# Kernel optimization log

Hardware: AMD Instinct MI355X
Metric: run time of the kernel (lower is better)

## Reference

```python
import jax, jax.numpy as jnp
import numpy as np

B, D_IN, H, V, T = 8192, 2048, 1024, 6, 6  # batch, enc input, hidden, total_vocab, max_length
TAU = 1.0

def setup_inputs() -> dict:
    key = jax.random.key(0)
    ks = jax.random.split(key, 16)
    s = 0.02
    return {
        "x": jax.random.normal(ks[0], (B, D_IN), jnp.float32),
        "u_noise": jax.random.uniform(ks[1], (T, B, V), jnp.float32),
        "W_enc": jax.random.normal(ks[2], (D_IN, H), jnp.float32) * s,
        "b_enc": jnp.zeros((H,), jnp.float32),
        "start_embed": jax.random.normal(ks[3], (H,), jnp.float32) * 0.01,
        "W_tok": jax.random.normal(ks[4], (V, H), jnp.float32) * s,
        "b_tok": jnp.zeros((H,), jnp.float32),
        "Wz": jax.random.normal(ks[5], (2 * H, H), jnp.float32) * s,
        "bz": jnp.zeros((H,), jnp.float32),
        "Wr": jax.random.normal(ks[6], (2 * H, H), jnp.float32) * s,
        "br": jnp.zeros((H,), jnp.float32),
        "Wh": jax.random.normal(ks[7], (2 * H, H), jnp.float32) * s,
        "bh": jnp.zeros((H,), jnp.float32),
        "W_out": jax.random.normal(ks[8], (H, V), jnp.float32) * s,
        "b_out": jnp.zeros((V,), jnp.float32),
    }

def reference(x, u_noise, W_enc, b_enc, start_embed, W_tok, b_tok,
              Wz, bz, Wr, br, Wh, bh, W_out, b_out):
    eps = 1e-10
    # uniform -> Gumbel(0,1) noise, precomputed per step: (T, B, V)
    g_all = -jnp.log(-jnp.log(u_noise + eps) + eps)
    h0 = x @ W_enc + b_enc                                   # encoder: (B, H)
    batch = x.shape[0]
    prev0 = jnp.broadcast_to(start_embed, (batch, start_embed.shape[0]))
    rc0 = jnp.ones((batch, 1), x.dtype)                      # running continue mask
    nt0 = jnp.zeros((batch,), x.dtype)                       # differentiable token count

    def step(carry, g):
        h, prev, rc, nt = carry
        nt = nt + rc[:, 0]
        comb = jnp.concatenate([prev, h], axis=-1)           # (B, 2H)
        z = jax.nn.sigmoid(comb @ Wz + bz)
        r = jax.nn.sigmoid(comb @ Wr + br)
        comb_r = jnp.concatenate([prev, r * h], axis=-1)
        h_tilde = jnp.tanh(comb_r @ Wh + bh)
        h = (1 - z) * h + z * h_tilde                        # GRU update
        logits = h @ W_out + b_out                           # (B, V)
        # hard gumbel-softmax with straight-through estimator
        y_soft = jax.nn.softmax((logits + g) / TAU, axis=-1)
        y_hard = jax.nn.one_hot(jnp.argmax(y_soft, axis=-1), logits.shape[-1],
                                dtype=logits.dtype)
        token = y_hard - jax.lax.stop_gradient(y_soft) + y_soft
        masked = token * rc                                  # zero out after STOP
        rc = rc * (1 - token[:, -1:])                        # STOP is last symbol
        prev = token @ W_tok + b_tok
        return (h, prev, rc, nt), (masked, logits)

    (_, _, _, n_tokens), (masked_seq, logits_seq) = jax.lax.scan(
        step, (h0, prev0, rc0, nt0), g_all)
    # (T, B, V) -> (B, T*V) message
    message = jnp.transpose(masked_seq, (1, 0, 2)).reshape(batch, -1)
    return message, logits_seq, n_tokens
```

## Files before the change

kernel.cpp:

```cpp
#include <hip/hip_runtime.h>
#include <math.h>

#define B_ 8192
#define DIN_ 2048
#define H_ 1024
#define V_ 6
#define T_ 6

typedef short bf16x8 __attribute__((ext_vector_type(8)));
typedef float f32x4 __attribute__((ext_vector_type(4)));

__device__ __forceinline__ unsigned short f32_bf16(float f) {
    unsigned u = __float_as_uint(f);
    u += 0x7FFFu + ((u >> 16) & 1u);
    return (unsigned short)(u >> 16);
}
__device__ __forceinline__ float bf16_f32(unsigned short h) {
    return __uint_as_float(((unsigned)h) << 16);
}
__device__ __forceinline__ float sigm_fast(float v) {
    return 1.0f / (1.0f + __expf(-v));
}
__device__ __forceinline__ float tanh_fast(float v) {
    return 1.0f - 2.0f / (1.0f + __expf(2.0f * v));
}

#define GLL16(g, l) __builtin_amdgcn_global_load_lds(                       \
        (const __attribute__((address_space(1))) void*)(g),                  \
        (__attribute__((address_space(3))) void*)(l), 16, 0, 0)

__global__ __launch_bounds__(256) void conv_w(const float* __restrict__ W,
        unsigned short* __restrict__ hi, unsigned short* __restrict__ lo)
{
    const int t = blockIdx.x * 256 + threadIdx.x;
    const int n = t & 1023;
    const int kb = t >> 10;
    unsigned hq[4], lq[4];
#pragma unroll
    for (int p = 0; p < 4; ++p) {
        const float v0 = W[(size_t)(kb * 8 + 2 * p) * 1024 + n];
        const float v1 = W[(size_t)(kb * 8 + 2 * p + 1) * 1024 + n];
        const unsigned short h0 = f32_bf16(v0), h1 = f32_bf16(v1);
        const unsigned short l0 = f32_bf16(v0 - bf16_f32(h0));
        const unsigned short l1 = f32_bf16(v1 - bf16_f32(h1));
        hq[p] = (unsigned)h0 | ((unsigned)h1 << 16);
        lq[p] = (unsigned)l0 | ((unsigned)l1 << 16);
    }
    const size_t c = ((size_t)(n >> 4) * 256 + kb) * 128 + (size_t)(n & 15) * 8;
    *(uint4*)(hi + c) = make_uint4(hq[0], hq[1], hq[2], hq[3]);
    *(uint4*)(lo + c) = make_uint4(lq[0], lq[1], lq[2], lq[3]);
}

__global__ __launch_bounds__(256) void conv_wb(const float* __restrict__ W,
        unsigned short* __restrict__ hi, unsigned short* __restrict__ lo)
{
    const int t = blockIdx.x * 256 + threadIdx.x;
    const int n = t & 1023;
    const int kb = t >> 10;
    unsigned hq[4], lq[4];
#pragma unroll
    for (int p = 0; p < 4; ++p) {
        const float v0 = W[(size_t)(1024 + kb * 8 + 2 * p) * 1024 + n];
        const float v1 = W[(size_t)(1024 + kb * 8 + 2 * p + 1) * 1024 + n];
        const unsigned short h0 = f32_bf16(v0), h1 = f32_bf16(v1);
        const unsigned short l0 = f32_bf16(v0 - bf16_f32(h0));
        const unsigned short l1 = f32_bf16(v1 - bf16_f32(h1));
        hq[p] = (unsigned)h0 | ((unsigned)h1 << 16);
        lq[p] = (unsigned)l0 | ((unsigned)l1 << 16);
    }
    const size_t c = ((size_t)(n >> 4) * 128 + kb) * 128 + (size_t)(n & 15) * 8;
    *(uint4*)(hi + c) = make_uint4(hq[0], hq[1], hq[2], hq[3]);
    *(uint4*)(lo + c) = make_uint4(lq[0], lq[1], lq[2], lq[3]);
}

__global__ __launch_bounds__(256) void conv_x(const float* __restrict__ X,
        unsigned short* __restrict__ hi, unsigned short* __restrict__ lo)
{
    const size_t t = (size_t)blockIdx.x * 256 + threadIdx.x;
    const int kb = (int)(t & 255);
    const int m = (int)(t >> 8);
    const float4 f0 = *(const float4*)(X + (size_t)m * 2048 + kb * 8);
    const float4 f1 = *(const float4*)(X + (size_t)m * 2048 + kb * 8 + 4);
    const float v[8] = {f0.x, f0.y, f0.z, f0.w, f1.x, f1.y, f1.z, f1.w};
    unsigned hq[4], lq[4];
#pragma unroll
    for (int p = 0; p < 4; ++p) {
        const unsigned short h0 = f32_bf16(v[2 * p]);
        const unsigned short h1 = f32_bf16(v[2 * p + 1]);
        const unsigned short l0 = f32_bf16(v[2 * p] - bf16_f32(h0));
        const unsigned short l1 = f32_bf16(v[2 * p + 1] - bf16_f32(h1));
        hq[p] = (unsigned)h0 | ((unsigned)h1 << 16);
        lq[p] = (unsigned)l0 | ((unsigned)l1 << 16);
    }
    const size_t c = ((size_t)(m >> 4) * 256 + kb) * 128 + (size_t)(m & 15) * 8;
    *(uint4*)(hi + c) = make_uint4(hq[0], hq[1], hq[2], hq[3]);
    *(uint4*)(lo + c) = make_uint4(lq[0], lq[1], lq[2], lq[3]);
}

__global__ __launch_bounds__(256) void prep_tables(
        const float* __restrict__ Wz, const float* __restrict__ Wr,
        const float* __restrict__ Wh,
        const float* __restrict__ bz, const float* __restrict__ br,
        const float* __restrict__ bh,
        const float* __restrict__ Wt, const float* __restrict__ bt,
        const float* __restrict__ se,
        float* __restrict__ Pz, float* __restrict__ Pr, float* __restrict__ Ph)
{
    __shared__ float emb[7][1024];
    const int tid = threadIdx.x;
    for (int i = tid; i < 7 * 1024; i += 256) {
        const int r = i >> 10, k = i & 1023;
        emb[r][k] = (r < 6) ? (Wt[(size_t)r * 1024 + k] + bt[k]) : se[k];
    }
    __syncthreads();
    const float* W = (blockIdx.y == 0) ? Wz : ((blockIdx.y == 1) ? Wr : Wh);
    const float* bb = (blockIdx.y == 0) ? bz : ((blockIdx.y == 1) ? br : bh);
    float* P = (blockIdx.y == 0) ? Pz : ((blockIdx.y == 1) ? Pr : Ph);
    const int n = blockIdx.x * 256 + tid;
    float acc[7] = {0.f, 0.f, 0.f, 0.f, 0.f, 0.f, 0.f};
    for (int k = 0; k < 1024; ++k) {
        const float wv = W[(size_t)k * 1024 + n];
#pragma unroll
        for (int r = 0; r < 7; ++r) acc[r] = fmaf(emb[r][k], wv, acc[r]);
    }
    const float bvv = bb[n];
#pragma unroll
    for (int r = 0; r < 7; ++r) P[(size_t)r * 1024 + n] = acc[r] + bvv;
}

__global__ __launch_bounds__(256) void init_misc(
        int* __restrict__ tokidx, float* __restrict__ rc, float* __restrict__ nt)
{
    const int t = blockIdx.x * 256 + threadIdx.x;
    tokidx[t] = 6;
    rc[t] = 1.0f;
    nt[t] = 0.0f;
}

__global__ __launch_bounds__(512, 3)
void gemm_bt(
    const unsigned short* __restrict__ A_hi, const unsigned short* __restrict__ A_lo,
    const unsigned short* __restrict__ B0_hi, const unsigned short* __restrict__ B0_lo,
    const unsigned short* __restrict__ B1_hi, const unsigned short* __restrict__ B1_lo,
    const float* __restrict__ P0, const float* __restrict__ P1,
    const int* __restrict__ tokidx,
    const float* __restrict__ zbuf, float* __restrict__ hbuf,
    float* __restrict__ outf,
    unsigned short* __restrict__ ophi, unsigned short* __restrict__ oplo,
    int nkb, int mode)
{
    __shared__ unsigned short lds[16384];

    const int tid = threadIdx.x;
    const int lane = tid & 63;
    const int w = tid >> 6;

    const int NX = gridDim.x;
    const int lin = blockIdx.y * NX + blockIdx.x;
    const int xcd = lin & 7;
    const int idx = lin >> 3;
    int bx = idx % NX;
    const int by = xcd * 8 + idx / NX;

    const unsigned short* Bhi = B0_hi;
    const unsigned short* Blo = B0_lo;
    const float* Pm = P0;
    int isR = 0;
    if (mode == 1 && bx >= 8) { bx -= 8; Bhi = B1_hi; Blo = B1_lo; Pm = P1; isR = 1; }

    const int m0 = by * 128;
    const int n0 = bx * 128;
    const int gma = by * 8 + w;
    const int gnb = bx * 8 + w;

    unsigned short* dAh = lds +          w * 512 + lane * 8;
    unsigned short* dAl = lds + 4096  +  w * 512 + lane * 8;
    unsigned short* dBh = lds + 8192  +  w * 512 + lane * 8;
    unsigned short* dBl = lds + 12288 +  w * 512 + lane * 8;

    f32x4 acc[2][4];
#pragma unroll
    for (int i = 0; i < 2; ++i)
#pragma unroll
        for (int j = 0; j < 4; ++j) acc[i][j] = (f32x4){0.f, 0.f, 0.f, 0.f};

    const int wr = w >> 1, wc = w & 1;
    const int fq = lane >> 4;
    const int fm = lane & 15;
    const int nsteps = nkb >> 2;

#pragma unroll 1
    for (int s = 0; s < nsteps; ++s) {
        __syncthreads();
        const size_t oa = ((size_t)gma * nkb + s * 4) * 128 + lane * 8;
        GLL16(A_hi + oa, dAh); GLL16(A_lo + oa, dAl);
        const size_t ob = ((size_t)gnb * nkb + s * 4) * 128 + lane * 8;
        GLL16(Bhi + ob, dBh); GLL16(Blo + ob, dBl);
        __syncthreads();

        bf16x8 ah[2], al[2];
#pragma unroll
        for (int i = 0; i < 2; ++i) {
            const int ra = (wr * 2 + i) * 512 + fq * 128 + fm * 8;
            ah[i] = *(const bf16x8*)(lds + ra);
            al[i] = *(const bf16x8*)(lds + 4096 + ra);
        }
#pragma unroll
        for (int j = 0; j < 4; ++j) {
            const int rb = (wc * 4 + j) * 512 + fq * 128 + fm * 8;
            const bf16x8 bh = *(const bf16x8*)(lds + 8192 + rb);
            const bf16x8 bl = *(const bf16x8*)(lds + 12288 + rb);
#pragma unroll
            for (int i = 0; i < 2; ++i) {
                acc[i][j] = __builtin_amdgcn_mfma_f32_16x16x32_bf16(ah[i], bh, acc[i][j], 0, 0, 0);
                acc[i][j] = __builtin_amdgcn_mfma_f32_16x16x32_bf16(ah[i], bl, acc[i][j], 0, 0, 0);
                acc[i][j] = __builtin_amdgcn_mfma_f32_16x16x32_bf16(al[i], bh, acc[i][j], 0, 0, 0);
            }
        }
    }

#pragma unroll
    for (int i = 0; i < 2; ++i) {
        int toks[4];
#pragma unroll
        for (int r = 0; r < 4; ++r) {
            const int row = m0 + wr * 32 + i * 16 + fq * 4 + r;
            toks[r] = tokidx ? tokidx[row] : 0;
        }
#pragma unroll
        for (int j = 0; j < 4; ++j) {
            const int col = n0 + wc * 64 + j * 16 + fm;
#pragma unroll
            for (int r = 0; r < 4; ++r) {
                const int row = m0 + wr * 32 + i * 16 + fq * 4 + r;
                const float v = acc[i][j][r] + Pm[(size_t)toks[r] * 1024 + col];
                const size_t off = (size_t)row * 1024 + col;
                const size_t pc = ((size_t)(row >> 4) * 128 + (col >> 3)) * 128
                                  + (size_t)(row & 15) * 8 + (col & 7);
                if (mode == 0) {
                    hbuf[off] = v;
                    const unsigned short hv = f32_bf16(v);
                    ophi[pc] = hv;
                    oplo[pc] = f32_bf16(v - bf16_f32(hv));
                } else if (mode == 1) {
                    const float sg = sigm_fast(v);
                    if (!isR) {
                        outf[off] = sg;
                    } else {
                        const float rh = sg * hbuf[off];
                        const unsigned short hv = f32_bf16(rh);
                        ophi[pc] = hv;
                        oplo[pc] = f32_bf16(rh - bf16_f32(hv));
                    }
                } else {
                    const float tv = tanh_fast(v);
                    const float zv = zbuf[off];
                    const float hn = (1.0f - zv) * hbuf[off] + zv * tv;
                    hbuf[off] = hn;
                    const unsigned short hv = f32_bf16(hn);
                    ophi[pc] = hv;
                    oplo[pc] = f32_bf16(hn - bf16_f32(hv));
                }
            }
        }
    }
}

__global__ __launch_bounds__(256)
void step_tok(const float* __restrict__ h,
              const float* __restrict__ W_out, const float* __restrict__ b_out,
              const float* __restrict__ u,
              float* __restrict__ rc, float* __restrict__ nt,
              int* __restrict__ tokidx,
              float* __restrict__ out_msg, float* __restrict__ out_logits,
              float* __restrict__ out_nt, int t)
{
    const int lane = threadIdx.x & 63;
    const int wv = threadIdx.x >> 6;
    const int b = blockIdx.x * 4 + wv;

    const float* hr = h + (size_t)b * H_;
    float s[6] = {0.f, 0.f, 0.f, 0.f, 0.f, 0.f};
#pragma unroll
    for (int i = 0; i < 4; ++i) {
        const int k0 = i * 256 + lane * 4;
        const float4 hv = *(const float4*)(hr + k0);
        const float he[4] = {hv.x, hv.y, hv.z, hv.w};
#pragma unroll
        for (int e = 0; e < 4; ++e) {
            const float* wp = W_out + (size_t)(k0 + e) * V_;
            const float xv = he[e];
#pragma unroll
            for (int v = 0; v < 6; ++v) s[v] = fmaf(xv, wp[v], s[v]);
        }
    }
#pragma unroll
    for (int m = 1; m < 64; m <<= 1) {
#pragma unroll
        for (int v = 0; v < 6; ++v) s[v] += __shfl_xor(s[v], m, 64);
    }

    float lg[6];
#pragma unroll
    for (int v = 0; v < 6; ++v) lg[v] = s[v] + b_out[v];

    const float* ub = u + (size_t)b * V_;
    const float eps = 1e-10f;
    float aa[6];
#pragma unroll
    for (int v = 0; v < 6; ++v) {
        const float g = -logf(-logf(ub[v] + eps) + eps);
        aa[v] = lg[v] + g;
    }
    int tok = 0;
    float best = aa[0];
#pragma unroll
    for (int v = 1; v < 6; ++v)
        if (aa[v] > best) { best = aa[v]; tok = v; }

    if (lane == 0) {
        const float rco = rc[b];
#pragma unroll
        for (int v = 0; v < 6; ++v) out_logits[(size_t)b * 6 + v] = lg[v];
#pragma unroll
        for (int v = 0; v < 6; ++v)
            out_msg[(size_t)b * 36 + t * 6 + v] = (v == tok) ? rco : 0.0f;
        const float ntn = nt[b] + rco;
        nt[b] = ntn;
        out_nt[b] = ntn;
        rc[b] = (tok == 5) ? 0.0f : rco;
        tokidx[b] = tok;
    }
}

extern "C" void kernel_launch(void* const* d_in, const int* in_sizes, int n_in,
                              void* d_out, int out_size, void* d_ws, size_t ws_size,
                              hipStream_t stream)
{
    (void)in_sizes; (void)n_in; (void)out_size; (void)ws_size;
    const float* x       = (const float*)d_in[0];
    const float* u_noise = (const float*)d_in[1];
    const float* W_enc   = (const float*)d_in[2];
    const float* b_enc   = (const float*)d_in[3];
    const float* start_e = (const float*)d_in[4];
    const float* W_tok   = (const float*)d_in[5];
    const float* b_tok   = (const float*)d_in[6];
    const float* Wz      = (const float*)d_in[7];
    const float* bz      = (const float*)d_in[8];
    const float* Wr      = (const float*)d_in[9];
    const float* br      = (const float*)d_in[10];
    const float* Wh      = (const float*)d_in[11];
    const float* bh      = (const float*)d_in[12];
    const float* W_out   = (const float*)d_in[13];
    const float* b_out   = (const float*)d_in[14];

    float* out = (float*)d_out;
    float* out_msg = out;
    float* out_logits = out + (size_t)B_ * T_ * V_;
    float* out_nt = out_logits + (size_t)T_ * B_ * V_;

    char* wsb = (char*)d_ws;
    const size_t MB = 1024 * 1024;
    unsigned short* wzb_hi = (unsigned short*)(wsb + 0 * MB);
    unsigned short* wzb_lo = (unsigned short*)(wsb + 2 * MB);
    unsigned short* wrb_hi = (unsigned short*)(wsb + 4 * MB);
    unsigned short* wrb_lo = (unsigned short*)(wsb + 6 * MB);
    unsigned short* whb_hi = (unsigned short*)(wsb + 8 * MB);
    unsigned short* whb_lo = (unsigned short*)(wsb + 10 * MB);
    unsigned short* we_hi  = (unsigned short*)(wsb + 12 * MB);
    unsigned short* we_lo  = (unsigned short*)(wsb + 16 * MB);
    unsigned short* x_hi   = (unsigned short*)(wsb + 20 * MB);
    unsigned short* x_lo   = (unsigned short*)(wsb + 52 * MB);
    float*  zbuf  = (float*)(wsb + 20 * MB);
    unsigned short* rh_hi  = (unsigned short*)(wsb + 52 * MB);
    unsigned short* rh_lo  = (unsigned short*)(wsb + 68 * MB);
    float*  hbuf  = (float*)(wsb + 84 * MB);
    unsigned short* h_hi   = (unsigned short*)(wsb + 116 * MB);
    unsigned short* h_lo   = (unsigned short*)(wsb + 132 * MB);
    float* Pz = (float*)(wsb + 148 * MB);
    float* Pr = Pz + 7 * 1024;
    float* Ph = Pr + 7 * 1024;
    int* tokidx = (int*)(Ph + 7 * 1024);
    float* rcb = (float*)(tokidx + B_);
    float* ntb = rcb + B_;

    conv_wb<<<512, 256, 0, stream>>>(Wz, wzb_hi, wzb_lo);
    conv_wb<<<512, 256, 0, stream>>>(Wr, wrb_hi, wrb_lo);
    conv_wb<<<512, 256, 0, stream>>>(Wh, whb_hi, whb_lo);
    conv_w<<<1024, 256, 0, stream>>>(W_enc, we_hi, we_lo);
    conv_x<<<8192, 256, 0, stream>>>(x, x_hi, x_lo);
    prep_tables<<<dim3(4, 3), 256, 0, stream>>>(Wz, Wr, Wh, bz, br, bh,
                                                W_tok, b_tok, start_e, Pz, Pr, Ph);
    init_misc<<<32, 256, 0, stream>>>(tokidx, rcb, ntb);

    gemm_bt<<<dim3(8, 64), 512, 0, stream>>>(
        x_hi, x_lo, we_hi, we_lo, nullptr, nullptr,
        b_enc, nullptr, nullptr,
        nullptr, hbuf, nullptr, h_hi, h_lo, 256, 0);

    for (int t = 0; t < T_; ++t) {
        gemm_bt<<<dim3(16, 64), 512, 0, stream>>>(
            h_hi, h_lo, wzb_hi, wzb_lo, wrb_hi, wrb_lo,
            Pz, Pr, tokidx,
            nullptr, hbuf, zbuf, rh_hi, rh_lo, 128, 1);
        gemm_bt<<<dim3(8, 64), 512, 0, stream>>>(
            rh_hi, rh_lo, whb_hi, whb_lo, nullptr, nullptr,
            Ph, nullptr, tokidx,
            zbuf, hbuf, nullptr, h_hi, h_lo, 128, 2);
        step_tok<<<B_ / 4, 256, 0, stream>>>(
            hbuf, W_out, b_out, u_noise + (size_t)t * B_ * V_,
            rcb, ntb, tokidx, out_msg,
            out_logits + (size_t)t * B_ * V_, out_nt, t);
    }
}
```

Baseline: 1.621 ms.

## Use 256x128 tile GEMM with XCD-aware block mapping for z/r gates

Adds a specialized gemm_big kernel for the fused z/r gate GEMM. It uses 256-row by 128-col tiles, where each wave computes a 64x64 block. Blocks are remapped so consecutive blocks on the same XCD share A rows. The goal is more operand reuse per LDS load and better L2 locality, at the cost of fewer blocks (512 vs 1024) and higher register pressure.

```diff
diff --git a/kernel.cpp b/kernel.cpp
--- a/kernel.cpp
+++ b/kernel.cpp
@@ -266,6 +266,126 @@
     }
 }
 
+__global__ __launch_bounds__(512, 4)
+void gemm_big(
+    const unsigned short* __restrict__ A_hi, const unsigned short* __restrict__ A_lo,
+    const unsigned short* __restrict__ B0_hi, const unsigned short* __restrict__ B0_lo,
+    const unsigned short* __restrict__ B1_hi, const unsigned short* __restrict__ B1_lo,
+    const float* __restrict__ P0, const float* __restrict__ P1,
+    const int* __restrict__ tokidx,
+    const float* __restrict__ hbuf, float* __restrict__ zbuf,
+    unsigned short* __restrict__ ophi, unsigned short* __restrict__ oplo,
+    int nkb)
+{
+    __shared__ unsigned short lds[24576];
+
+    const int tid = threadIdx.x;
+    const int lane = tid & 63;
+    const int w = tid >> 6;
+
+    const int NX = gridDim.x;
+    const int lin = blockIdx.y * NX + blockIdx.x;
+    const int xcd = lin & 7;
+    const int idx = lin >> 3;
+    int bx = idx % NX;
+    const int by = xcd * 4 + idx / NX;
+
+    const unsigned short* Bhi = B0_hi;
+    const unsigned short* Blo = B0_lo;
+    const float* Pm = P0;
+    int isR = 0;
+    if (bx >= 8) { bx -= 8; Bhi = B1_hi; Blo = B1_lo; Pm = P1; isR = 1; }
+
+    const int m0 = by * 256;
+    const int n0 = bx * 128;
+    const int mg0 = by * 16;
+    const int ng0 = bx * 8;
+
+    const int pa = w >> 2;
+    const int ga0 = (w & 3) * 4;
+    const int gb0 = (w & 3) * 2;
+    const unsigned short* Asrc = pa ? A_lo : A_hi;
+    const unsigned short* Bsrc = pa ? Blo : Bhi;
+
+    f32x4 acc[4][4];
+#pragma unroll
+    for (int i = 0; i < 4; ++i)
+#pragma unroll
+        for (int j = 0; j < 4; ++j) acc[i][j] = (f32x4){0.f, 0.f, 0.f, 0.f};
+
+    const int wr = w >> 1, wc = w & 1;
+    const int fq = lane >> 4;
+    const int fm = lane & 15;
+    const int nsteps = nkb >> 2;
+
+#pragma unroll 1
+    for (int s = 0; s < nsteps; ++s) {
+        __syncthreads();
+#pragma unroll
+        for (int q = 0; q < 4; ++q) {
+            const size_t so = ((size_t)(mg0 + ga0 + q) * nkb + s * 4) * 128 + lane * 8;
+            GLL16(Asrc + so, lds + pa * 8192 + (ga0 + q) * 512 + lane * 8);
+        }
+#pragma unroll
+        for (int q = 0; q < 2; ++q) {
+            const size_t so = ((size_t)(ng0 + gb0 + q) * nkb + s * 4) * 128 + lane * 8;
+            GLL16(Bsrc + so, lds + 16384 + pa * 4096 + (gb0 + q) * 512 + lane * 8);
+        }
+        __syncthreads();
+
+        bf16x8 ah[4], al[4];
+#pragma unroll
+        for (int i = 0; i < 4; ++i) {
+            const int ra = (wr * 4 + i) * 512 + fq * 128 + fm * 8;
+            ah[i] = *(const bf16x8*)(lds + ra);
+            al[i] = *(const bf16x8*)(lds + 8192 + ra);
+        }
+#pragma unroll
+        for (int j = 0; j < 4; ++j) {
+            const int rb = 16384 + (wc * 4 + j) * 512 + fq * 128 + fm * 8;
+            const bf16x8 bh = *(const bf16x8*)(lds + rb);
+            const bf16x8 bl = *(const bf16x8*)(lds + rb + 4096);
+#pragma unroll
+            for (int i = 0; i < 4; ++i) {
+                acc[i][j] = __builtin_amdgcn_mfma_f32_16x16x32_bf16(ah[i], bh, acc[i][j], 0, 0, 0);
+                acc[i][j] = __builtin_amdgcn_mfma_f32_16x16x32_bf16(ah[i], bl, acc[i][j], 0, 0, 0);
+                acc[i][j] = __builtin_amdgcn_mfma_f32_16x16x32_bf16(al[i], bh, acc[i][j], 0, 0, 0);
+            }
+        }
+    }
+
+#pragma unroll
+    for (int i = 0; i < 4; ++i) {
+        int toks[4];
+#pragma unroll
+        for (int r = 0; r < 4; ++r) {
+            const int row = m0 + wr * 64 + i * 16 + fq * 4 + r;
+            toks[r] = tokidx[row];
+        }
+#pragma unroll
+        for (int j = 0; j < 4; ++j) {
+            const int col = n0 + wc * 64 + j * 16 + fm;
+#pragma unroll
+            for (int r = 0; r < 4; ++r) {
+                const int row = m0 + wr * 64 + i * 16 + fq * 4 + r;
+                const float v = acc[i][j][r] + Pm[(size_t)toks[r] * 1024 + col];
+                const size_t off = (size_t)row * 1024 + col;
+                const float sg = sigm_fast(v);
+                if (!isR) {
+                    zbuf[off] = sg;
+                } else {
+                    const size_t pc = ((size_t)(row >> 4) * 128 + (col >> 3)) * 128
+                                      + (size_t)(row & 15) * 8 + (col & 7);
+                    const float rh = sg * hbuf[off];
+                    const unsigned short hv = f32_bf16(rh);
+                    ophi[pc] = hv;
+                    oplo[pc] = f32_bf16(rh - bf16_f32(hv));
+                }
+            }
+        }
+    }
+}
+
 __global__ __launch_bounds__(256)
 void step_tok(const float* __restrict__ h,
               const float* __restrict__ W_out, const float* __restrict__ b_out,
@@ -399,10 +519,10 @@
         nullptr, hbuf, nullptr, h_hi, h_lo, 256, 0);
 
     for (int t = 0; t < T_; ++t) {
-        gemm_bt<<<dim3(16, 64), 512, 0, stream>>>(
+        gemm_big<<<dim3(16, 32), 512, 0, stream>>>(
             h_hi, h_lo, wzb_hi, wzb_lo, wrb_hi, wrb_lo,
             Pz, Pr, tokidx,
-            nullptr, hbuf, zbuf, rh_hi, rh_lo, 128, 1);
+            hbuf, zbuf, rh_hi, rh_lo, 128);
         gemm_bt<<<dim3(8, 64), 512, 0, stream>>>(
             rh_hi, rh_lo, whb_hi, whb_lo, nullptr, nullptr,
             Ph, nullptr, tokidx,
```

After: 1.763 ms. 1.09x slower.

## Double-buffer LDS in GEMM to overlap global loads with MFMA compute

Applied to the files above, without the earlier changes.

Doubles the shared-memory tile buffer and restructures the K loop into a ping-pong schedule, issuing the next tile's global-to-LDS loads before computing on the current tile. This halves the barriers per step and hides load latency behind the matrix instructions. The larger LDS footprint may reduce the number of resident blocks per CU, and the unrolled-by-two loop assumes an even step count.

```diff
diff --git a/kernel.cpp b/kernel.cpp
--- a/kernel.cpp
+++ b/kernel.cpp
@@ -149,7 +149,7 @@
     unsigned short* __restrict__ ophi, unsigned short* __restrict__ oplo,
     int nkb, int mode)
 {
-    __shared__ unsigned short lds[16384];
+    __shared__ unsigned short lds[32768];
 
     const int tid = threadIdx.x;
     const int lane = tid & 63;
@@ -173,10 +173,8 @@
     const int gma = by * 8 + w;
     const int gnb = bx * 8 + w;
 
-    unsigned short* dAh = lds +          w * 512 + lane * 8;
-    unsigned short* dAl = lds + 4096  +  w * 512 + lane * 8;
-    unsigned short* dBh = lds + 8192  +  w * 512 + lane * 8;
-    unsigned short* dBl = lds + 12288 +  w * 512 + lane * 8;
+    const int dA = w * 512 + lane * 8;
+    const int dB = 8192 + w * 512 + lane * 8;
 
     f32x4 acc[2][4];
 #pragma unroll
@@ -189,35 +187,61 @@
     const int fm = lane & 15;
     const int nsteps = nkb >> 2;
 
+    const unsigned short* pAh = A_hi + (size_t)gma * nkb * 128 + lane * 8;
+    const unsigned short* pAl = A_lo + (size_t)gma * nkb * 128 + lane * 8;
+    const unsigned short* pBh = Bhi + (size_t)gnb * nkb * 128 + lane * 8;
+    const unsigned short* pBl = Blo + (size_t)gnb * nkb * 128 + lane * 8;
+
+    unsigned short* const L0 = lds;
+    unsigned short* const L1 = lds + 16384;
+
+#define STAGE_TO(dst_) do {                                                    \
+    GLL16(pAh, (dst_) + dA); GLL16(pAl, (dst_) + 4096 + dA);                   \
+    GLL16(pBh, (dst_) + dB); GLL16(pBl, (dst_) + 4096 + dB);                   \
+    pAh += 512; pAl += 512; pBh += 512; pBl += 512;                            \
+} while (0)
+
+#define COMPUTE_FROM(cb_) do {                                                 \
+    bf16x8 ah[2], al[2];                                                       \
+    _Pragma("unroll")                                                          \
+    for (int i = 0; i < 2; ++i) {                                              \
+        const int ra = (wr * 2 + i) * 512 + fq * 128 + fm * 8;                 \
+        ah[i] = *(const bf16x8*)((cb_) + ra);                                  \
+        al[i] = *(const bf16x8*)((cb_) + 4096 + ra);                           \
+    }                                                                          \
+    _Pragma("unroll")                                                          \
+    for (int j = 0; j < 4; ++j) {                                              \
+        const int rb = 8192 + (wc * 4 + j) * 512 + fq * 128 + fm * 8;          \
+        const bf16x8 bh = *(const bf16x8*)((cb_) + rb);                        \
+        const bf16x8 bl = *(const bf16x8*)((cb_) + 4096 + rb);                 \
+        _Pragma("unroll")                                                      \
+        for (int i = 0; i < 2; ++i) {                                          \
+            acc[i][j] = __builtin_amdgcn_mfma_f32_16x16x32_bf16(ah[i], bh, acc[i][j], 0, 0, 0); \
+            acc[i][j] = __builtin_amdgcn_mfma_f32_16x16x32_bf16(ah[i], bl, acc[i][j], 0, 0, 0); \
+            acc[i][j] = __builtin_amdgcn_mfma_f32_16x16x32_bf16(al[i], bh, acc[i][j], 0, 0, 0); \
+        }                                                                      \
+    }                                                                          \
+} while (0)
+
+    STAGE_TO(L0);
+    __syncthreads();
+
 #pragma unroll 1
-    for (int s = 0; s < nsteps; ++s) {
+    for (int s = 0; s < nsteps - 2; s += 2) {
+        STAGE_TO(L1);
+        COMPUTE_FROM(L0);
         __syncthreads();
-        const size_t oa = ((size_t)gma * nkb + s * 4) * 128 + lane * 8;
-        GLL16(A_hi + oa, dAh); GLL16(A_lo + oa, dAl);
-        const size_t ob = ((size_t)gnb * nkb + s * 4) * 128 + lane * 8;
-        GLL16(Bhi + ob, dBh); GLL16(Blo + ob, dBl);
+        STAGE_TO(L0);
+        COMPUTE_FROM(L1);
         __syncthreads();
-
-        bf16x8 ah[2], al[2];
-#pragma unroll
-        for (int i = 0; i < 2; ++i) {
-            const int ra = (wr * 2 + i) * 512 + fq * 128 + fm * 8;
-            ah[i] = *(const bf16x8*)(lds + ra);
-            al[i] = *(const bf16x8*)(lds + 4096 + ra);
-        }
-#pragma unroll
-        for (int j = 0; j < 4; ++j) {
-            const int rb = (wc * 4 + j) * 512 + fq * 128 + fm * 8;
-            const bf16x8 bh = *(const bf16x8*)(lds + 8192 + rb);
-            const bf16x8 bl = *(const bf16x8*)(lds + 12288 + rb);
-#pragma unroll
-            for (int i = 0; i < 2; ++i) {
-                acc[i][j] = __builtin_amdgcn_mfma_f32_16x16x32_bf16(ah[i], bh, acc[i][j], 0, 0, 0);
-                acc[i][j] = __builtin_amdgcn_mfma_f32_16x16x32_bf16(ah[i], bl, acc[i][j], 0, 0, 0);
-                acc[i][j] = __builtin_amdgcn_mfma_f32_16x16x32_bf16(al[i], bh, acc[i][j], 0, 0, 0);
-            }
-        }
-    }
+    }
+    STAGE_TO(L1);
+    COMPUTE_FROM(L0);
+    __syncthreads();
+    COMPUTE_FROM(L1);
+
+#undef STAGE_TO
+#undef COMPUTE_FROM
 
 #pragma unroll
     for (int i = 0; i < 2; ++i) {
```

Result: no change. 1.605 ms (-1.0%).
